# Kernel tuning notes

Hardware: AMD Instinct MI355X
Metric: run time of the kernel (lower is better)

Reference implementation:

```python
import jax, jax.numpy as jnp
import numpy as np

C = 128
EPS = 1e-5


def _layernorm(x, w, b):
    m = jnp.mean(x, axis=-1, keepdims=True)
    v = jnp.mean(jnp.square(x - m), axis=-1, keepdims=True)
    return (x - m) * jax.lax.rsqrt(v + EPS) * w + b


def _linear(x, w, b):
    # torch Linear: y = x @ W.T + b, W is [out, in]
    return jnp.einsum('bijc,dc->bijd', x, w) + b


def setup_inputs() -> dict:
    key = jax.random.key(0)
    ks = jax.random.split(key, 8)
    B, N = 1, 384
    z = jax.random.normal(ks[0], (B, N, N, C), dtype=jnp.float32)
    pair_mask = jnp.ones((B, N, N), dtype=jnp.float32)
    def W(k):
        return jax.random.normal(k, (C, C), dtype=jnp.float32) * 0.02
    return {
        'z': z,
        'pair_mask': pair_mask,
        'ln_in_w': jnp.ones((C,), jnp.float32),
        'ln_in_b': jnp.zeros((C,), jnp.float32),
        'ln_out_w': jnp.ones((C,), jnp.float32),
        'ln_out_b': jnp.zeros((C,), jnp.float32),
        'proj_a_w': W(ks[1]), 'proj_a_b': jnp.zeros((C,), jnp.float32),
        'gate_a_w': W(ks[2]), 'gate_a_b': jnp.zeros((C,), jnp.float32),
        'proj_b_w': W(ks[3]), 'proj_b_b': jnp.zeros((C,), jnp.float32),
        'gate_b_w': W(ks[4]), 'gate_b_b': jnp.zeros((C,), jnp.float32),
        'gate_o_w': W(ks[5]), 'gate_o_b': jnp.zeros((C,), jnp.float32),
        'proj_o_w': W(ks[6]), 'proj_o_b': jnp.zeros((C,), jnp.float32),
    }


def reference(z, pair_mask, ln_in_w, ln_in_b, ln_out_w, ln_out_b,
              proj_a_w, proj_a_b, gate_a_w, gate_a_b,
              proj_b_w, proj_b_b, gate_b_w, gate_b_b,
              gate_o_w, gate_o_b, proj_o_w, proj_o_b):
    mask = pair_mask[..., None]                     # [B,N,N,1]
    z_norm = _layernorm(z, ln_in_w, ln_in_b)
    gate = jax.nn.sigmoid(_linear(z_norm, gate_o_w, gate_o_b))
    a = _linear(z_norm, proj_a_w, proj_a_b) * jax.nn.sigmoid(_linear(z_norm, gate_a_w, gate_a_b)) * mask
    b = _linear(z_norm, proj_b_w, proj_b_b) * jax.nn.sigmoid(_linear(z_norm, gate_b_w, gate_b_b)) * mask
    # incoming: out[i,j,c] = sum_k a[k,j,c] * b[k,i,c]
    contracted = jnp.einsum('bkjc,bkic->bijc', a, b)
    contracted = contracted * mask
    out = _linear(_layernorm(contracted, ln_out_w, ln_out_b), proj_o_w, proj_o_b)
    return out * gate
```

## Files before the change

kernel.cpp:

```cpp
#include <hip/hip_runtime.h>
#include <math.h>

#define NN 384
#define CC 128
#define MT (NN * NN)

typedef __attribute__((ext_vector_type(8))) short bf16x8;
typedef __attribute__((ext_vector_type(4))) short short4v;
typedef __attribute__((ext_vector_type(4))) float f32x4;

__device__ __forceinline__ float bf2f(short u) {
  union { float f; unsigned i; } v; v.i = ((unsigned)(unsigned short)u) << 16; return v.f;
}
__device__ __forceinline__ short f2bf(float f) {
  union { float f; unsigned i; } v; v.f = f;
  unsigned x = v.i;
  return (short)((x + 0x7fffu + ((x >> 16) & 1u)) >> 16);
}
__device__ __forceinline__ void cp16(void* lds, const void* g) {
  __builtin_amdgcn_global_load_lds(
      (const __attribute__((address_space(1))) void*)g,
      (__attribute__((address_space(3))) void*)lds, 16, 0, 0);
}
__device__ __forceinline__ float sigm(float x) { return 1.f / (1.f + __expf(-x)); }


__global__ __launch_bounds__(256) void k_wts(
    const float* __restrict__ w0, const float* __restrict__ w1,
    const float* __restrict__ w2, const float* __restrict__ w3,
    const float* __restrict__ w4, const float* __restrict__ w5,
    short* __restrict__ out)
{
  int idx = blockIdx.x * 256 + threadIdx.x;
  const float* s;
  switch (idx >> 14) {
    case 0: s = w0; break; case 1: s = w1; break; case 2: s = w2; break;
    case 3: s = w3; break; case 4: s = w4; break; default: s = w5; break;
  }
  out[idx] = f2bf(s[idx & 16383]);
}

__global__ __launch_bounds__(256) void k_ln_in(
    const float* __restrict__ z, const float* __restrict__ lw,
    const float* __restrict__ lb, short* __restrict__ zn)
{
  const int wid = threadIdx.x >> 6, lane = threadIdx.x & 63;
  const size_t p = (size_t)blockIdx.x * 4 + wid;
  const float2 v = ((const float2*)(z + p * CC))[lane];
  float s = v.x + v.y, sq = v.x * v.x + v.y * v.y;
  #pragma unroll
  for (int o = 32; o > 0; o >>= 1) { s += __shfl_xor(s, o); sq += __shfl_xor(sq, o); }
  const float mu = s * (1.f / 128.f);
  const float rstd = rsqrtf(sq * (1.f / 128.f) - mu * mu + 1e-5f);
  const float2 w2 = ((const float2*)lw)[lane];
  const float2 b2 = ((const float2*)lb)[lane];
  short2 o2;
  o2.x = f2bf((v.x - mu) * rstd * w2.x + b2.x);
  o2.y = f2bf((v.y - mu) * rstd * w2.y + b2.y);
  ((short2*)(zn + p * CC))[lane] = o2;
}

template<bool PAIRED>
__global__ __launch_bounds__(256) void k_lin(
    const short* __restrict__ zn, const short* __restrict__ Bw,
    const float* __restrict__ bias_p, const float* __restrict__ bias_g,
    const float* __restrict__ mask, short* __restrict__ outp)
{
  __shared__ char smem[PAIRED ? 49152 : 34816];
  __shared__ float mask_s[128];
  short* As = (short*)smem;
  short* Bs = (short*)(smem + 16384);
  short* T  = (short*)smem;

  const int tid = threadIdx.x, wid = tid >> 6, lane = tid & 63;
  const int tile = blockIdx.x;
  const int y0 = tile / 3, x0 = (tile % 3) * 128, p0 = tile * 128;

  if (PAIRED && tid < 128) mask_s[tid] = mask[(size_t)(x0 + tid) * NN + y0];

  f32x4 accP[4][4], accG[4][4];
  #pragma unroll
  for (int i = 0; i < 4; ++i) {
    #pragma unroll
    for (int j = 0; j < 4; ++j) {
      accP[i][j] = f32x4{0.f, 0.f, 0.f, 0.f};
      accG[i][j] = f32x4{0.f, 0.f, 0.f, 0.f};
    }
  }
  const int wm = (wid >> 1) * 64, wn = (wid & 1) * 64;
  const int slot = (lane & 7) ^ (lane >> 3);

  #pragma unroll
  for (int kk = 0; kk < 2; ++kk) {
    __syncthreads();
    #pragma unroll
    for (int i = 0; i < 4; ++i) {
      const int rbase = (i * 4 + wid) * 8;
      const int r = rbase + (lane >> 3);
      const size_t srow = PAIRED ? ((size_t)(x0 + r) * NN + y0) : (size_t)(p0 + r);
      cp16((char*)As + rbase * 128,
           (const char*)(zn + srow * CC) + kk * 128 + slot * 16);
    }
    const int NR = PAIRED ? 8 : 4;
    #pragma unroll
    for (int i = 0; i < NR; ++i) {
      const int rbase = (i * 4 + wid) * 8;
      const int r = rbase + (lane >> 3);
      cp16((char*)Bs + rbase * 128,
           (const char*)(Bw + (size_t)r * CC) + kk * 128 + slot * 16);
    }
    __syncthreads();
    #pragma unroll
    for (int ks = 0; ks < 2; ++ks) {
      const int u = ks * 4 + (lane >> 4);
      const int sl = (u ^ (lane & 7)) * 8;
      bf16x8 a[4], bp[4], bg[4];
      #pragma unroll
      for (int f = 0; f < 4; ++f)
        a[f] = *(const bf16x8*)&As[(wm + f * 16 + (lane & 15)) * 64 + sl];
      #pragma unroll
      for (int f = 0; f < 4; ++f)
        bp[f] = *(const bf16x8*)&Bs[(wn + f * 16 + (lane & 15)) * 64 + sl];
      if (PAIRED) {
        #pragma unroll
        for (int f = 0; f < 4; ++f)
          bg[f] = *(const bf16x8*)&Bs[128 * 64 + (wn + f * 16 + (lane & 15)) * 64 + sl];
      }
      #pragma unroll
      for (int fm = 0; fm < 4; ++fm) {
        #pragma unroll
        for (int fn = 0; fn < 4; ++fn) {
          accP[fm][fn] = __builtin_amdgcn_mfma_f32_16x16x32_bf16(a[fm], bp[fn], accP[fm][fn], 0, 0, 0);
          if (PAIRED)
            accG[fm][fn] = __builtin_amdgcn_mfma_f32_16x16x32_bf16(a[fm], bg[fn], accG[fm][fn], 0, 0, 0);
        }
      }
    }
  }

  __syncthreads();
  #pragma unroll
  for (int fm = 0; fm < 4; ++fm) {
    #pragma unroll
    for (int fn = 0; fn < 4; ++fn) {
      const int c = wn + fn * 16 + (lane & 15);
      const int mb = wm + fm * 16 + (lane >> 4) * 4;
      const float bpv = bias_p[c];
      if (PAIRED) {
        const float bgv = bias_g[c];
        short4v st;
        #pragma unroll
        for (int e = 0; e < 4; ++e) {
          const float pv = accP[fm][fn][e] + bpv;
          const float gv = accG[fm][fn][e] + bgv;
          st[e] = f2bf(pv * sigm(gv) * mask_s[mb + e]);
        }
        *(short4v*)&T[c * 136 + mb] = st;
      } else {
        #pragma unroll
        for (int e = 0; e < 4; ++e)
          T[(mb + e) * 136 + c] = f2bf(sigm(accP[fm][fn][e] + bpv));
      }
    }
  }
  __syncthreads();
  const size_t rowoff = (size_t)y0 * NN + x0;
  #pragma unroll
  for (int rep = 0; rep < 8; ++rep) {
    const int row = rep * 16 + (tid >> 4), chunk = tid & 15;
    const bf16x8 v = *(const bf16x8*)&T[row * 136 + chunk * 8];
    if (PAIRED)
      *(bf16x8*)(outp + (size_t)row * MT + rowoff + chunk * 8) = v;
    else
      *(bf16x8*)(outp + (size_t)(p0 + row) * CC + chunk * 8) = v;
  }
}

__global__ __launch_bounds__(256) void k_tri(
    const short* __restrict__ wsa, const short* __restrict__ wsb,
    const float* __restrict__ mask, short* __restrict__ wsct)
{
  __shared__ char smem[34816];
  short* As = (short*)smem;
  short* Bs = (short*)(smem + 16384);
  short* T  = (short*)smem;

  const int tid = threadIdx.x, wid = tid >> 6, lane = tid & 63;
  const int o = (blockIdx.x & 7) * 144 + (blockIdx.x >> 3);
  const int c = o / 9, t9 = o % 9;
  const int i0 = (t9 / 3) * 128, j0 = (t9 % 3) * 128;
  const short* Ab = wsa + (size_t)c * MT;
  const short* Bb = wsb + (size_t)c * MT;

  f32x4 acc[4][4];
  #pragma unroll
  for (int i = 0; i < 4; ++i) {
    #pragma unroll
    for (int j = 0; j < 4; ++j) acc[i][j] = f32x4{0.f, 0.f, 0.f, 0.f};
  }
  const int wm = (wid >> 1) * 64, wn = (wid & 1) * 64;
  const int slot = (lane & 7) ^ (lane >> 3);

  for (int kt = 0; kt < 6; ++kt) {
    __syncthreads();
    #pragma unroll
    for (int i = 0; i < 4; ++i) {
      const int rbase = (i * 4 + wid) * 8;
      const int r = rbase + (lane >> 3);
      cp16((char*)As + rbase * 128,
           (const char*)(Ab + (size_t)(j0 + r) * NN) + kt * 128 + slot * 16);
      cp16((char*)Bs + rbase * 128,
           (const char*)(Bb + (size_t)(i0 + r) * NN) + kt * 128 + slot * 16);
    }
    __syncthreads();
    #pragma unroll
    for (int ks = 0; ks < 2; ++ks) {
      const int u = ks * 4 + (lane >> 4);
      const int sl = (u ^ (lane & 7)) * 8;
      bf16x8 a[4], b[4];
      #pragma unroll
      for (int f = 0; f < 4; ++f) {
        a[f] = *(const bf16x8*)&As[(wm + f * 16 + (lane & 15)) * 64 + sl];
        b[f] = *(const bf16x8*)&Bs[(wn + f * 16 + (lane & 15)) * 64 + sl];
      }
      #pragma unroll
      for (int fm = 0; fm < 4; ++fm) {
        #pragma unroll
        for (int fn = 0; fn < 4; ++fn)
          acc[fm][fn] = __builtin_amdgcn_mfma_f32_16x16x32_bf16(a[fm], b[fn], acc[fm][fn], 0, 0, 0);
      }
    }
  }

  __syncthreads();
  #pragma unroll
  for (int fm = 0; fm < 4; ++fm) {
    #pragma unroll
    for (int fn = 0; fn < 4; ++fn) {
      const int il = wn + fn * 16 + (lane & 15);
      const int jb = wm + fm * 16 + (lane >> 4) * 4;
      const f32x4 mk = *(const f32x4*)(mask + (size_t)(i0 + il) * NN + j0 + jb);
      short4v st;
      #pragma unroll
      for (int e = 0; e < 4; ++e) st[e] = f2bf(acc[fm][fn][e] * mk[e]);
      *(short4v*)&T[il * 136 + jb] = st;
    }
  }
  __syncthreads();
  #pragma unroll
  for (int rep = 0; rep < 8; ++rep) {
    const int row = rep * 16 + (tid >> 4), chunk = tid & 15;
    const bf16x8 v = *(const bf16x8*)&T[row * 136 + chunk * 8];
    *(bf16x8*)(wsct + (size_t)c * MT + (size_t)(i0 + row) * NN + j0 + chunk * 8) = v;
  }
}

__global__ __launch_bounds__(256) void k_ln_out(
    const short* __restrict__ wsct, const float* __restrict__ lw,
    const float* __restrict__ lb, short* __restrict__ z2)
{
  __shared__ float T[128][65];
  const int tid = threadIdx.x;
  const int p0 = blockIdx.x * 64;

  #pragma unroll
  for (int rep = 0; rep < 4; ++rep) {
    const int c = rep * 32 + (tid >> 3);
    const int pp = (tid & 7) * 8;
    const bf16x8 v = *(const bf16x8*)(wsct + (size_t)c * MT + p0 + pp);
    #pragma unroll
    for (int e = 0; e < 8; ++e) T[c][pp + e] = bf2f(v[e]);
  }
  __syncthreads();

  const int pl = tid >> 2, q = tid & 3;
  float s = 0.f, sq = 0.f;
  #pragma unroll
  for (int ccd = 0; ccd < 32; ++ccd) {
    const float v = T[q * 32 + ccd][pl];
    s += v; sq += v * v;
  }
  s += __shfl_xor(s, 1); sq += __shfl_xor(sq, 1);
  s += __shfl_xor(s, 2); sq += __shfl_xor(sq, 2);
  const float mu = s * (1.f / 128.f);
  const float rstd = rsqrtf(sq * (1.f / 128.f) - mu * mu + 1e-5f);

  const size_t p = p0 + pl;
  #pragma unroll
  for (int v8 = 0; v8 < 4; ++v8) {
    const int cb = q * 32 + v8 * 8;
    bf16x8 st;
    #pragma unroll
    for (int e = 0; e < 8; ++e)
      st[e] = f2bf((T[cb + e][pl] - mu) * rstd * lw[cb + e] + lb[cb + e]);
    *(bf16x8*)(z2 + p * CC + cb) = st;
  }
}

__global__ __launch_bounds__(256) void k_out(
    const short* __restrict__ z2, const short* __restrict__ Bw,
    const float* __restrict__ bo, const short* __restrict__ gate,
    float* __restrict__ out)
{
  __shared__ short As[128 * 64], Bs[128 * 64];
  const int tid = threadIdx.x, wid = tid >> 6, lane = tid & 63;
  const int p0 = blockIdx.x * 128;

  f32x4 acc[4][4];
  #pragma unroll
  for (int i = 0; i < 4; ++i) {
    #pragma unroll
    for (int j = 0; j < 4; ++j) acc[i][j] = f32x4{0.f, 0.f, 0.f, 0.f};
  }
  const int wm = (wid >> 1) * 64, wn = (wid & 1) * 64;
  const int slot = (lane & 7) ^ (lane >> 3);

  #pragma unroll
  for (int kk = 0; kk < 2; ++kk) {
    __syncthreads();
    #pragma unroll
    for (int i = 0; i < 4; ++i) {
      const int rbase = (i * 4 + wid) * 8;
      const int r = rbase + (lane >> 3);
      cp16((char*)As + rbase * 128,
           (const char*)(z2 + (size_t)(p0 + r) * CC) + kk * 128 + slot * 16);
      cp16((char*)Bs + rbase * 128,
           (const char*)(Bw + (size_t)r * CC) + kk * 128 + slot * 16);
    }
    __syncthreads();
    #pragma unroll
    for (int ks = 0; ks < 2; ++ks) {
      const int u = ks * 4 + (lane >> 4);
      const int sl = (u ^ (lane & 7)) * 8;
      bf16x8 a[4], b[4];
      #pragma unroll
      for (int f = 0; f < 4; ++f) {
        a[f] = *(const bf16x8*)&As[(wm + f * 16 + (lane & 15)) * 64 + sl];
        b[f] = *(const bf16x8*)&Bs[(wn + f * 16 + (lane & 15)) * 64 + sl];
      }
      #pragma unroll
      for (int fm = 0; fm < 4; ++fm) {
        #pragma unroll
        for (int fn = 0; fn < 4; ++fn)
          acc[fm][fn] = __builtin_amdgcn_mfma_f32_16x16x32_bf16(a[fm], b[fn], acc[fm][fn], 0, 0, 0);
      }
    }
  }
  #pragma unroll
  for (int fm = 0; fm < 4; ++fm) {
    #pragma unroll
    for (int fn = 0; fn < 4; ++fn) {
      const int d = wn + fn * 16 + (lane & 15);
      const int mb = wm + fm * 16 + (lane >> 4) * 4;
      const float bd = bo[d];
      #pragma unroll
      for (int e = 0; e < 4; ++e) {
        const float g = bf2f(gate[(size_t)(p0 + mb + e) * CC + d]);
        out[(size_t)(p0 + mb + e) * CC + d] = (acc[fm][fn][e] + bd) * g;
      }
    }
  }
}

extern "C" void kernel_launch(void* const* d_in, const int* in_sizes, int n_in,
                              void* d_out, int out_size, void* d_ws, size_t ws_size,
                              hipStream_t stream) {
  const float* z        = (const float*)d_in[0];
  const float* mask     = (const float*)d_in[1];
  const float* ln_in_w  = (const float*)d_in[2];
  const float* ln_in_b  = (const float*)d_in[3];
  const float* ln_out_w = (const float*)d_in[4];
  const float* ln_out_b = (const float*)d_in[5];
  const float* pa_w = (const float*)d_in[6];  const float* pa_b = (const float*)d_in[7];
  const float* ga_w = (const float*)d_in[8];  const float* ga_b = (const float*)d_in[9];
  const float* pb_w = (const float*)d_in[10]; const float* pb_b = (const float*)d_in[11];
  const float* gb_w = (const float*)d_in[12]; const float* gb_b = (const float*)d_in[13];
  const float* go_w = (const float*)d_in[14]; const float* go_b = (const float*)d_in[15];
  const float* po_w = (const float*)d_in[16]; const float* po_b = (const float*)d_in[17];

  char* ws = (char*)d_ws;
  const size_t SZ = (size_t)MT * CC * 2;
  short* zn   = (short*)(ws);
  short* wsa  = (short*)(ws + SZ);
  short* wsb  = (short*)(ws + 2 * SZ);
  short* wsg  = (short*)(ws + 3 * SZ);
  short* wts  = (short*)(ws + 4 * SZ);
  short* wsct = zn;
  short* z2   = wsa;

  k_wts<<<384, 256, 0, stream>>>(pa_w, ga_w, pb_w, gb_w, go_w, po_w, wts);
  k_ln_in<<<MT / 4, 256, 0, stream>>>(z, ln_in_w, ln_in_b, zn);
  k_lin<true ><<<1152, 256, 0, stream>>>(zn, wts,             pa_b, ga_b, mask, wsa);
  k_lin<true ><<<1152, 256, 0, stream>>>(zn, wts + 2 * 16384, pb_b, gb_b, mask, wsb);
  k_lin<false><<<1152, 256, 0, stream>>>(zn, wts + 4 * 16384, go_b, nullptr, nullptr, wsg);
  k_tri<<<1152, 256, 0, stream>>>(wsa, wsb, mask, wsct);
  k_ln_out<<<MT / 64, 256, 0, stream>>>(wsct, ln_out_w, ln_out_b, z2);
  k_out<<<1152, 256, 0, stream>>>(z2, wts + 5 * 16384, po_b, wsg, (float*)d_out);
}
```

Baseline: 354.9 us.

## Fuse output layernorm, output projection and gate GEMM into one final kernel

Removes the separate gate linear pass and the k_ln_out/k_out kernels. A new k_fin kernel loads the contracted tile, applies the output layernorm in LDS, and runs two GEMMs: the output projection on the normalized tile and the gate projection on the input-normalized activations. It then applies the sigmoid gate in the epilogue. This avoids writing and re-reading the gate tensor and the intermediate z2 and saves two launches, at the cost of 80KB LDS per block, which lowers occupancy, and a separate workspace buffer for wsct.

```diff
diff --git a/kernel.cpp b/kernel.cpp
--- a/kernel.cpp
+++ b/kernel.cpp
@@ -60,13 +60,12 @@
   ((short2*)(zn + p * CC))[lane] = o2;
 }
 
-template<bool PAIRED>
 __global__ __launch_bounds__(256) void k_lin(
     const short* __restrict__ zn, const short* __restrict__ Bw,
     const float* __restrict__ bias_p, const float* __restrict__ bias_g,
     const float* __restrict__ mask, short* __restrict__ outp)
 {
-  __shared__ char smem[PAIRED ? 49152 : 34816];
+  __shared__ char smem[49152];
   __shared__ float mask_s[128];
   short* As = (short*)smem;
   short* Bs = (short*)(smem + 16384);
@@ -74,9 +73,9 @@
 
   const int tid = threadIdx.x, wid = tid >> 6, lane = tid & 63;
   const int tile = blockIdx.x;
-  const int y0 = tile / 3, x0 = (tile % 3) * 128, p0 = tile * 128;
-
-  if (PAIRED && tid < 128) mask_s[tid] = mask[(size_t)(x0 + tid) * NN + y0];
+  const int y0 = tile / 3, x0 = (tile % 3) * 128;
+
+  if (tid < 128) mask_s[tid] = mask[(size_t)(x0 + tid) * NN + y0];
 
   f32x4 accP[4][4], accG[4][4];
   #pragma unroll
@@ -97,13 +96,11 @@
     for (int i = 0; i < 4; ++i) {
       const int rbase = (i * 4 + wid) * 8;
       const int r = rbase + (lane >> 3);
-      const size_t srow = PAIRED ? ((size_t)(x0 + r) * NN + y0) : (size_t)(p0 + r);
       cp16((char*)As + rbase * 128,
-           (const char*)(zn + srow * CC) + kk * 128 + slot * 16);
-    }
-    const int NR = PAIRED ? 8 : 4;
-    #pragma unroll
-    for (int i = 0; i < NR; ++i) {
+           (const char*)(zn + ((size_t)(x0 + r) * NN + y0) * CC) + kk * 128 + slot * 16);
+    }
+    #pragma unroll
+    for (int i = 0; i < 8; ++i) {
       const int rbase = (i * 4 + wid) * 8;
       const int r = rbase + (lane >> 3);
       cp16((char*)Bs + rbase * 128,
@@ -116,23 +113,17 @@
       const int sl = (u ^ (lane & 7)) * 8;
       bf16x8 a[4], bp[4], bg[4];
       #pragma unroll
-      for (int f = 0; f < 4; ++f)
-        a[f] = *(const bf16x8*)&As[(wm + f * 16 + (lane & 15)) * 64 + sl];
-      #pragma unroll
-      for (int f = 0; f < 4; ++f)
+      for (int f = 0; f < 4; ++f) {
+        a[f]  = *(const bf16x8*)&As[(wm + f * 16 + (lane & 15)) * 64 + sl];
         bp[f] = *(const bf16x8*)&Bs[(wn + f * 16 + (lane & 15)) * 64 + sl];
-      if (PAIRED) {
-        #pragma unroll
-        for (int f = 0; f < 4; ++f)
-          bg[f] = *(const bf16x8*)&Bs[128 * 64 + (wn + f * 16 + (lane & 15)) * 64 + sl];
+        bg[f] = *(const bf16x8*)&Bs[128 * 64 + (wn + f * 16 + (lane & 15)) * 64 + sl];
       }
       #pragma unroll
       for (int fm = 0; fm < 4; ++fm) {
         #pragma unroll
         for (int fn = 0; fn < 4; ++fn) {
           accP[fm][fn] = __builtin_amdgcn_mfma_f32_16x16x32_bf16(a[fm], bp[fn], accP[fm][fn], 0, 0, 0);
-          if (PAIRED)
-            accG[fm][fn] = __builtin_amdgcn_mfma_f32_16x16x32_bf16(a[fm], bg[fn], accG[fm][fn], 0, 0, 0);
+          accG[fm][fn] = __builtin_amdgcn_mfma_f32_16x16x32_bf16(a[fm], bg[fn], accG[fm][fn], 0, 0, 0);
         }
       }
     }
@@ -146,21 +137,15 @@
       const int c = wn + fn * 16 + (lane & 15);
       const int mb = wm + fm * 16 + (lane >> 4) * 4;
       const float bpv = bias_p[c];
-      if (PAIRED) {
-        const float bgv = bias_g[c];
-        short4v st;
-        #pragma unroll
-        for (int e = 0; e < 4; ++e) {
-          const float pv = accP[fm][fn][e] + bpv;
-          const float gv = accG[fm][fn][e] + bgv;
-          st[e] = f2bf(pv * sigm(gv) * mask_s[mb + e]);
-        }
-        *(short4v*)&T[c * 136 + mb] = st;
-      } else {
-        #pragma unroll
-        for (int e = 0; e < 4; ++e)
-          T[(mb + e) * 136 + c] = f2bf(sigm(accP[fm][fn][e] + bpv));
-      }
+      const float bgv = bias_g[c];
+      short4v st;
+      #pragma unroll
+      for (int e = 0; e < 4; ++e) {
+        const float pv = accP[fm][fn][e] + bpv;
+        const float gv = accG[fm][fn][e] + bgv;
+        st[e] = f2bf(pv * sigm(gv) * mask_s[mb + e]);
+      }
+      *(short4v*)&T[c * 136 + mb] = st;
     }
   }
   __syncthreads();
@@ -169,10 +154,7 @@
   for (int rep = 0; rep < 8; ++rep) {
     const int row = rep * 16 + (tid >> 4), chunk = tid & 15;
     const bf16x8 v = *(const bf16x8*)&T[row * 136 + chunk * 8];
-    if (PAIRED)
-      *(bf16x8*)(outp + (size_t)row * MT + rowoff + chunk * 8) = v;
-    else
-      *(bf16x8*)(outp + (size_t)(p0 + row) * CC + chunk * 8) = v;
+    *(bf16x8*)(outp + (size_t)row * MT + rowoff + chunk * 8) = v;
   }
 }
 
@@ -255,62 +237,66 @@
   }
 }
 
-__global__ __launch_bounds__(256) void k_ln_out(
-    const short* __restrict__ wsct, const float* __restrict__ lw,
-    const float* __restrict__ lb, short* __restrict__ z2)
-{
-  __shared__ float T[128][65];
-  const int tid = threadIdx.x;
-  const int p0 = blockIdx.x * 64;
-
-  #pragma unroll
-  for (int rep = 0; rep < 4; ++rep) {
-    const int c = rep * 32 + (tid >> 3);
-    const int pp = (tid & 7) * 8;
-    const bf16x8 v = *(const bf16x8*)(wsct + (size_t)c * MT + p0 + pp);
-    #pragma unroll
-    for (int e = 0; e < 8; ++e) T[c][pp + e] = bf2f(v[e]);
-  }
-  __syncthreads();
-
-  const int pl = tid >> 2, q = tid & 3;
+__global__ __launch_bounds__(256) void k_fin(
+    const short* __restrict__ wsct, const short* __restrict__ zn,
+    const short* __restrict__ wpo, const short* __restrict__ wgo,
+    const float* __restrict__ lw, const float* __restrict__ lb,
+    const float* __restrict__ po_b, const float* __restrict__ go_b,
+    float* __restrict__ out)
+{
+  __shared__ char smem[81920];
+  short* Tt    = (short*)smem;
+  float* lnw_s = (float*)(smem + 34816);
+  float* lnb_s = (float*)(smem + 35328);
+  short* As2   = (short*)smem;
+  short* Bs    = (short*)(smem + 16384);
+  short* A1    = (short*)(smem + 49152);
+
+  const int tid = threadIdx.x, wid = tid >> 6, lane = tid & 63;
+  const size_t p0 = (size_t)blockIdx.x * 128;
+
+  #pragma unroll
+  for (int rep = 0; rep < 8; ++rep) {
+    const int c = rep * 16 + (tid >> 4), chunk = tid & 15;
+    const bf16x8 v = *(const bf16x8*)(wsct + (size_t)c * MT + p0 + chunk * 8);
+    *(bf16x8*)&Tt[c * 136 + chunk * 8] = v;
+  }
+  if (tid < 128) { lnw_s[tid] = lw[tid]; lnb_s[tid] = lb[tid]; }
+  __syncthreads();
+
+  const int pl = tid >> 1, q = tid & 1;
   float s = 0.f, sq = 0.f;
   #pragma unroll
-  for (int ccd = 0; ccd < 32; ++ccd) {
-    const float v = T[q * 32 + ccd][pl];
+  for (int cc = 0; cc < 64; ++cc) {
+    const float v = bf2f(Tt[(q * 64 + cc) * 136 + pl]);
     s += v; sq += v * v;
   }
   s += __shfl_xor(s, 1); sq += __shfl_xor(sq, 1);
-  s += __shfl_xor(s, 2); sq += __shfl_xor(sq, 2);
   const float mu = s * (1.f / 128.f);
   const float rstd = rsqrtf(sq * (1.f / 128.f) - mu * mu + 1e-5f);
 
-  const size_t p = p0 + pl;
-  #pragma unroll
-  for (int v8 = 0; v8 < 4; ++v8) {
-    const int cb = q * 32 + v8 * 8;
+  #pragma unroll
+  for (int cb = 0; cb < 8; ++cb) {
+    const int c0 = q * 64 + cb * 8;
     bf16x8 st;
     #pragma unroll
-    for (int e = 0; e < 8; ++e)
-      st[e] = f2bf((T[cb + e][pl] - mu) * rstd * lw[cb + e] + lb[cb + e]);
-    *(bf16x8*)(z2 + p * CC + cb) = st;
-  }
-}
-
-__global__ __launch_bounds__(256) void k_out(
-    const short* __restrict__ z2, const short* __restrict__ Bw,
-    const float* __restrict__ bo, const short* __restrict__ gate,
-    float* __restrict__ out)
-{
-  __shared__ short As[128 * 64], Bs[128 * 64];
-  const int tid = threadIdx.x, wid = tid >> 6, lane = tid & 63;
-  const int p0 = blockIdx.x * 128;
-
-  f32x4 acc[4][4];
+    for (int e = 0; e < 8; ++e) {
+      const int c = c0 + e;
+      st[e] = f2bf((bf2f(Tt[c * 136 + pl]) - mu) * rstd * lnw_s[c] + lnb_s[c]);
+    }
+    const int slotg = q * 8 + cb;
+    const int kk = slotg >> 3, s3 = slotg & 7;
+    *(bf16x8*)&A1[kk * 8192 + pl * 64 + (s3 ^ (pl & 7)) * 8] = st;
+  }
+
+  f32x4 accO[4][4], accG[4][4];
   #pragma unroll
   for (int i = 0; i < 4; ++i) {
     #pragma unroll
-    for (int j = 0; j < 4; ++j) acc[i][j] = f32x4{0.f, 0.f, 0.f, 0.f};
+    for (int j = 0; j < 4; ++j) {
+      accO[i][j] = f32x4{0.f, 0.f, 0.f, 0.f};
+      accG[i][j] = f32x4{0.f, 0.f, 0.f, 0.f};
+    }
   }
   const int wm = (wid >> 1) * 64, wn = (wid & 1) * 64;
   const int slot = (lane & 7) ^ (lane >> 3);
@@ -322,41 +308,57 @@
     for (int i = 0; i < 4; ++i) {
       const int rbase = (i * 4 + wid) * 8;
       const int r = rbase + (lane >> 3);
-      cp16((char*)As + rbase * 128,
-           (const char*)(z2 + (size_t)(p0 + r) * CC) + kk * 128 + slot * 16);
-      cp16((char*)Bs + rbase * 128,
-           (const char*)(Bw + (size_t)r * CC) + kk * 128 + slot * 16);
+      cp16((char*)As2 + rbase * 128,
+           (const char*)(zn + (p0 + r) * CC) + kk * 128 + slot * 16);
+    }
+    #pragma unroll
+    for (int i = 0; i < 8; ++i) {
+      const int rbase = (i * 4 + wid) * 8;
+      const int r = rbase + (lane >> 3);
+      const short* wrow = (r < 128) ? (wpo + (size_t)r * CC) : (wgo + (size_t)(r - 128) * CC);
+      cp16((char*)Bs + rbase * 128, (const char*)wrow + kk * 128 + slot * 16);
     }
     __syncthreads();
     #pragma unroll
     for (int ks = 0; ks < 2; ++ks) {
       const int u = ks * 4 + (lane >> 4);
       const int sl = (u ^ (lane & 7)) * 8;
-      bf16x8 a[4], b[4];
+      bf16x8 a1[4], a2[4], bo[4], bg[4];
       #pragma unroll
       for (int f = 0; f < 4; ++f) {
-        a[f] = *(const bf16x8*)&As[(wm + f * 16 + (lane & 15)) * 64 + sl];
-        b[f] = *(const bf16x8*)&Bs[(wn + f * 16 + (lane & 15)) * 64 + sl];
+        const int row = wm + f * 16 + (lane & 15);
+        a1[f] = *(const bf16x8*)&A1[kk * 8192 + row * 64 + sl];
+        a2[f] = *(const bf16x8*)&As2[row * 64 + sl];
+      }
+      #pragma unroll
+      for (int f = 0; f < 4; ++f) {
+        const int row = wn + f * 16 + (lane & 15);
+        bo[f] = *(const bf16x8*)&Bs[row * 64 + sl];
+        bg[f] = *(const bf16x8*)&Bs[(128 + row) * 64 + sl];
       }
       #pragma unroll
       for (int fm = 0; fm < 4; ++fm) {
         #pragma unroll
-        for (int fn = 0; fn < 4; ++fn)
-          acc[fm][fn] = __builtin_amdgcn_mfma_f32_16x16x32_bf16(a[fm], b[fn], acc[fm][fn], 0, 0, 0);
-      }
-    }
-  }
+        for (int fn = 0; fn < 4; ++fn) {
+          accO[fm][fn] = __builtin_amdgcn_mfma_f32_16x16x32_bf16(a1[fm], bo[fn], accO[fm][fn], 0, 0, 0);
+          accG[fm][fn] = __builtin_amdgcn_mfma_f32_16x16x32_bf16(a2[fm], bg[fn], accG[fm][fn], 0, 0, 0);
+        }
+      }
+    }
+  }
+
   #pragma unroll
   for (int fm = 0; fm < 4; ++fm) {
     #pragma unroll
     for (int fn = 0; fn < 4; ++fn) {
       const int d = wn + fn * 16 + (lane & 15);
       const int mb = wm + fm * 16 + (lane >> 4) * 4;
-      const float bd = bo[d];
+      const float bd = po_b[d];
+      const float gd = go_b[d];
       #pragma unroll
       for (int e = 0; e < 4; ++e) {
-        const float g = bf2f(gate[(size_t)(p0 + mb + e) * CC + d]);
-        out[(size_t)(p0 + mb + e) * CC + d] = (acc[fm][fn][e] + bd) * g;
+        const float g = sigm(accG[fm][fn][e] + gd);
+        out[(p0 + mb + e) * CC + d] = (accO[fm][fn][e] + bd) * g;
       }
     }
   }
@@ -383,17 +385,14 @@
   short* zn   = (short*)(ws);
   short* wsa  = (short*)(ws + SZ);
   short* wsb  = (short*)(ws + 2 * SZ);
-  short* wsg  = (short*)(ws + 3 * SZ);
+  short* wsct = (short*)(ws + 3 * SZ);
   short* wts  = (short*)(ws + 4 * SZ);
-  short* wsct = zn;
-  short* z2   = wsa;
 
   k_wts<<<384, 256, 0, stream>>>(pa_w, ga_w, pb_w, gb_w, go_w, po_w, wts);
   k_ln_in<<<MT / 4, 256, 0, stream>>>(z, ln_in_w, ln_in_b, zn);
-  k_lin<true ><<<1152, 256, 0, stream>>>(zn, wts,             pa_b, ga_b, mask, wsa);
-  k_lin<true ><<<1152, 256, 0, stream>>>(zn, wts + 2 * 16384, pb_b, gb_b, mask, wsb);
-  k_lin<false><<<1152, 256, 0, stream>>>(zn, wts + 4 * 16384, go_b, nullptr, nullptr, wsg);
+  k_lin<<<1152, 256, 0, stream>>>(zn, wts,             pa_b, ga_b, mask, wsa);
+  k_lin<<<1152, 256, 0, stream>>>(zn, wts + 2 * 16384, pb_b, gb_b, mask, wsb);
   k_tri<<<1152, 256, 0, stream>>>(wsa, wsb, mask, wsct);
-  k_ln_out<<<MT / 64, 256, 0, stream>>>(wsct, ln_out_w, ln_out_b, z2);
-  k_out<<<1152, 256, 0, stream>>>(z2, wts + 5 * 16384, po_b, wsg, (float*)d_out);
-}
+  k_fin<<<1152, 256, 0, stream>>>(wsct, zn, wts + 5 * 16384, wts + 4 * 16384,
+                                  ln_out_w, ln_out_b, po_b, go_b, (float*)d_out);
+}
```

Result: faster. 329.2 us (-7.2%).
